# Kernel optimization log

Hardware: AMD Instinct MI355X
Metric: run time of the kernel (lower is better)

Reference implementation:

```python
import jax, jax.numpy as jnp
import numpy as np


def setup_inputs() -> dict:
    key = jax.random.key(0)
    k1, k2, k3 = jax.random.split(key, 3)
    B, N, L, H, E = 4, 4, 1024, 8, 64
    queries = jax.random.normal(k1, (B, N, L, H, E), dtype=jnp.float32)
    keys = jax.random.normal(k2, (B, N, L, H, E), dtype=jnp.float32)
    values = jax.random.normal(k3, (B, N, L, H, E), dtype=jnp.float32)
    return {"queries": queries, "keys": keys, "values": values}


def reference(queries, keys, values):
    B, N, L, H, E = queries.shape
    S = values.shape[2]
    scale = 1.0 / jnp.sqrt(jnp.asarray(E, queries.dtype))
    # scores: [B, N, H, L, S]
    scores = jnp.einsum('bnlhe,bnshe->bnhls', queries, keys)
    # causal mask: True above the diagonal (future positions), broadcast over b,n,h
    causal = jnp.triu(jnp.ones((L, S), dtype=bool), k=1)
    scores = jnp.where(causal, -jnp.inf, scores)
    A = jax.nn.softmax(scale * scores, axis=-1)  # dropout p=0.0 -> identity
    V = jnp.einsum('bnhls,bnshd->bnlhd', A, values)
    return V
```

## Files before the change

### kernel.cpp

```cpp
#include <hip/hip_runtime.h>
#include <hip/hip_bf16.h>


typedef __bf16 bf16x8 __attribute__((ext_vector_type(8)));
typedef float  f32x4  __attribute__((ext_vector_type(4)));

#define SEQ 1024
#define ROWSTRIDE 512
#define LDSPAD 72

__device__ inline bf16x8 pack8(float4 a, float4 b) {
    bf16x8 f;
    f[0]=(__bf16)a.x; f[1]=(__bf16)a.y; f[2]=(__bf16)a.z; f[3]=(__bf16)a.w;
    f[4]=(__bf16)b.x; f[5]=(__bf16)b.y; f[6]=(__bf16)b.z; f[7]=(__bf16)b.w;
    return f;
}

__device__ inline void lds_barrier() {
    asm volatile("s_waitcnt lgkmcnt(0)\n\ts_barrier" ::: "memory");
}

__global__ __launch_bounds__(256) void attn_fwd(
    const float* __restrict__ Qg,
    const float* __restrict__ Kg,
    const float* __restrict__ Vg,
    float* __restrict__ Og)
{
    __shared__ __bf16 Kds[64][LDSPAD];
    __shared__ __bf16 Vds[64][LDSPAD];
    __shared__ __bf16 Pds[2][4][16][LDSPAD];

    const int blk  = blockIdx.x;
    const int pr   = blk >> 7;
    const int head = blk & 127;
    const int h    = head & 7;
    const int bn   = head >> 3;
    const int qts[2] = { pr, 15 - pr };

    const int tid  = threadIdx.x;
    const int wave = tid >> 6;
    const int lane = tid & 63;
    const int quad = lane >> 4;
    const int l15  = lane & 15;

    const size_t base = (size_t)bn * SEQ * ROWSTRIDE + (size_t)h * 64;

    bf16x8 qa[2][2];
    int qrow[2];
    #pragma unroll
    for (int st = 0; st < 2; ++st) {
        qrow[st] = qts[st] * 64 + wave * 16;
        const float* qp = Qg + base + (size_t)(qrow[st] + l15) * ROWSTRIDE + quad * 8;
        #pragma unroll
        for (int t = 0; t < 2; ++t)
            qa[st][t] = pack8(*(const float4*)(qp + t * 32),
                              *(const float4*)(qp + t * 32 + 4));
    }

    f32x4 o[2][4];
    float lsum[2][4];
    #pragma unroll
    for (int st = 0; st < 2; ++st) {
        #pragma unroll
        for (int e = 0; e < 4; ++e) o[st][e] = (f32x4){0.f, 0.f, 0.f, 0.f};
        #pragma unroll
        for (int r = 0; r < 4; ++r) lsum[st][r] = 0.f;
    }

    const float kscale = 0.125f * 1.44269504088896f;

    const int sr = tid >> 2, sc = (tid & 3) << 4;
    const int ve = tid & 63, vs = (tid >> 6) << 4;

    const int ntiles = qts[1] + 1;

    const float* kbase = Kg + base;
    const float* vbase = Vg + base;

    float4 kpre[4];
    float  vpre[16];
    {
        const float* kp = kbase + (size_t)sr * ROWSTRIDE + sc;
        #pragma unroll
        for (int i = 0; i < 4; ++i) kpre[i] = *(const float4*)(kp + i * 4);
        const float* vp = vbase + (size_t)vs * ROWSTRIDE + ve;
        #pragma unroll
        for (int j = 0; j < 16; ++j) vpre[j] = vp[(size_t)j * ROWSTRIDE];
    }

    for (int tile = 0; tile < ntiles; ++tile) {
        lds_barrier();

        *(bf16x8*)&Kds[sr][sc]     = pack8(kpre[0], kpre[1]);
        *(bf16x8*)&Kds[sr][sc + 8] = pack8(kpre[2], kpre[3]);
        {
            bf16x8 f0, f1;
            #pragma unroll
            for (int jj = 0; jj < 8; ++jj) { f0[jj] = (__bf16)vpre[jj]; f1[jj] = (__bf16)vpre[8 + jj]; }
            *(bf16x8*)&Vds[ve][vs]     = f0;
            *(bf16x8*)&Vds[ve][vs + 8] = f1;
        }

        if (tile + 1 < ntiles) {
            const int s0n = (tile + 1) * 64;
            const float* kp = kbase + (size_t)(s0n + sr) * ROWSTRIDE + sc;
            #pragma unroll
            for (int i = 0; i < 4; ++i) kpre[i] = *(const float4*)(kp + i * 4);
            const float* vp = vbase + (size_t)(s0n + vs) * ROWSTRIDE + ve;
            #pragma unroll
            for (int j = 0; j < 16; ++j) vpre[j] = vp[(size_t)j * ROWSTRIDE];
        }

        lds_barrier();

        #pragma unroll
        for (int st = 0; st < 2; ++st) {
            if (tile > qts[st]) continue;
            f32x4 sacc[4];
            #pragma unroll
            for (int c = 0; c < 4; ++c) {
                sacc[c] = (f32x4){0.f, 0.f, 0.f, 0.f};
                #pragma unroll
                for (int t = 0; t < 2; ++t) {
                    bf16x8 kb = *(const bf16x8*)&Kds[c * 16 + l15][t * 32 + quad * 8];
                    sacc[c] = __builtin_amdgcn_mfma_f32_16x16x32_bf16(qa[st][t], kb, sacc[c], 0, 0, 0);
                }
            }
            const bool diag = (tile == qts[st]);
            #pragma unroll
            for (int c = 0; c < 4; ++c) {
                #pragma unroll
                for (int r = 0; r < 4; ++r) {
                    float x = sacc[c][r] * kscale;
                    if (diag && (c * 16 + l15 > wave * 16 + quad * 4 + r)) x = -1e30f;
                    float p = exp2f(x);
                    lsum[st][r] += p;
                    Pds[st][wave][quad * 4 + r][c * 16 + l15] = (__bf16)p;
                }
            }
        }

        asm volatile("s_waitcnt lgkmcnt(0)" ::: "memory");

        const bool both = (tile <= qts[0]);
        #pragma unroll
        for (int e = 0; e < 4; ++e) {
            #pragma unroll
            for (int t = 0; t < 2; ++t) {
                bf16x8 vb = *(const bf16x8*)&Vds[e * 16 + l15][t * 32 + quad * 8];
                if (both) {
                    bf16x8 pa0 = *(const bf16x8*)&Pds[0][wave][l15][t * 32 + quad * 8];
                    o[0][e] = __builtin_amdgcn_mfma_f32_16x16x32_bf16(pa0, vb, o[0][e], 0, 0, 0);
                }
                bf16x8 pa1 = *(const bf16x8*)&Pds[1][wave][l15][t * 32 + quad * 8];
                o[1][e] = __builtin_amdgcn_mfma_f32_16x16x32_bf16(pa1, vb, o[1][e], 0, 0, 0);
            }
        }
    }

    #pragma unroll
    for (int st = 0; st < 2; ++st) {
        float inv_l[4];
        #pragma unroll
        for (int r = 0; r < 4; ++r) {
            float s = lsum[st][r];
            #pragma unroll
            for (int off = 1; off < 16; off <<= 1)
                s += __shfl_xor(s, off);
            inv_l[r] = 1.f / s;
        }
        #pragma unroll
        for (int e = 0; e < 4; ++e) {
            #pragma unroll
            for (int r = 0; r < 4; ++r) {
                size_t oidx = base + (size_t)(qrow[st] + quad * 4 + r) * ROWSTRIDE + e * 16 + l15;
                Og[oidx] = o[st][e][r] * inv_l[r];
            }
        }
    }
}

extern "C" void kernel_launch(void* const* d_in, const int* in_sizes, int n_in,
                              void* d_out, int out_size, void* d_ws, size_t ws_size,
                              hipStream_t stream) {
    const float* Qg = (const float*)d_in[0];
    const float* Kg = (const float*)d_in[1];
    const float* Vg = (const float*)d_in[2];
    float* Og = (float*)d_out;
    attn_fwd<<<dim3(1024), dim3(256), 0, stream>>>(Qg, Kg, Vg, Og);
}
```

Measured before the change: 167.2 us.

## Transpose MFMA operands so each lane owns a query row, vectorize P and output stores

Swaps the A/B operands of both MFMAs so score and output accumulators are transposed, giving each lane a single query row. This lets P be written to LDS as 4-wide bf16 vectors, reduces the row-sum reduction to two shuffles, and turns output stores into float4 writes. The softmax scale is folded into Q at load time and exp2 uses the raw hardware builtin, with masking applied after the exponent. The cost is slightly different rounding from scaling Q before the bf16 conversion, and LDS bank patterns change for the vector P writes.

```diff
diff --git a/kernel.cpp b/kernel.cpp
--- a/kernel.cpp
+++ b/kernel.cpp
@@ -3,6 +3,7 @@
 
 
 typedef __bf16 bf16x8 __attribute__((ext_vector_type(8)));
+typedef __bf16 bf16x4 __attribute__((ext_vector_type(4)));
 typedef float  f32x4  __attribute__((ext_vector_type(4)));
 
 #define SEQ 1024
@@ -13,6 +14,13 @@
     bf16x8 f;
     f[0]=(__bf16)a.x; f[1]=(__bf16)a.y; f[2]=(__bf16)a.z; f[3]=(__bf16)a.w;
     f[4]=(__bf16)b.x; f[5]=(__bf16)b.y; f[6]=(__bf16)b.z; f[7]=(__bf16)b.w;
+    return f;
+}
+
+__device__ inline bf16x8 pack8s(float4 a, float4 b, float s) {
+    bf16x8 f;
+    f[0]=(__bf16)(a.x*s); f[1]=(__bf16)(a.y*s); f[2]=(__bf16)(a.z*s); f[3]=(__bf16)(a.w*s);
+    f[4]=(__bf16)(b.x*s); f[5]=(__bf16)(b.y*s); f[6]=(__bf16)(b.z*s); f[7]=(__bf16)(b.w*s);
     return f;
 }
 
@@ -45,6 +53,8 @@
 
     const size_t base = (size_t)bn * SEQ * ROWSTRIDE + (size_t)h * 64;
 
+    const float kscale = 0.125f * 1.44269504088896f;
+
     bf16x8 qa[2][2];
     int qrow[2];
     #pragma unroll
@@ -53,21 +63,18 @@
         const float* qp = Qg + base + (size_t)(qrow[st] + l15) * ROWSTRIDE + quad * 8;
         #pragma unroll
         for (int t = 0; t < 2; ++t)
-            qa[st][t] = pack8(*(const float4*)(qp + t * 32),
-                              *(const float4*)(qp + t * 32 + 4));
+            qa[st][t] = pack8s(*(const float4*)(qp + t * 32),
+                               *(const float4*)(qp + t * 32 + 4), kscale);
     }
 
     f32x4 o[2][4];
-    float lsum[2][4];
+    float lsum[2];
     #pragma unroll
     for (int st = 0; st < 2; ++st) {
         #pragma unroll
         for (int e = 0; e < 4; ++e) o[st][e] = (f32x4){0.f, 0.f, 0.f, 0.f};
-        #pragma unroll
-        for (int r = 0; r < 4; ++r) lsum[st][r] = 0.f;
+        lsum[st] = 0.f;
     }
-
-    const float kscale = 0.125f * 1.44269504088896f;
 
     const int sr = tid >> 2, sc = (tid & 3) << 4;
     const int ve = tid & 63, vs = (tid >> 6) << 4;
@@ -123,21 +130,25 @@
                 #pragma unroll
                 for (int t = 0; t < 2; ++t) {
                     bf16x8 kb = *(const bf16x8*)&Kds[c * 16 + l15][t * 32 + quad * 8];
-                    sacc[c] = __builtin_amdgcn_mfma_f32_16x16x32_bf16(qa[st][t], kb, sacc[c], 0, 0, 0);
+                    sacc[c] = __builtin_amdgcn_mfma_f32_16x16x32_bf16(kb, qa[st][t], sacc[c], 0, 0, 0);
                 }
             }
             const bool diag = (tile == qts[st]);
+            const int qin = wave * 16 + l15;
+            float ls = 0.f;
             #pragma unroll
             for (int c = 0; c < 4; ++c) {
+                bf16x4 pk;
                 #pragma unroll
                 for (int r = 0; r < 4; ++r) {
-                    float x = sacc[c][r] * kscale;
-                    if (diag && (c * 16 + l15 > wave * 16 + quad * 4 + r)) x = -1e30f;
-                    float p = exp2f(x);
-                    lsum[st][r] += p;
-                    Pds[st][wave][quad * 4 + r][c * 16 + l15] = (__bf16)p;
+                    float p = __builtin_amdgcn_exp2f(sacc[c][r]);
+                    if (diag && (c * 16 + quad * 4 + r > qin)) p = 0.f;
+                    ls += p;
+                    pk[r] = (__bf16)p;
                 }
+                *(bf16x4*)&Pds[st][wave][l15][c * 16 + quad * 4] = pk;
             }
+            lsum[st] += ls;
         }
 
         asm volatile("s_waitcnt lgkmcnt(0)" ::: "memory");
@@ -149,33 +160,30 @@
             for (int t = 0; t < 2; ++t) {
                 bf16x8 vb = *(const bf16x8*)&Vds[e * 16 + l15][t * 32 + quad * 8];
                 if (both) {
-                    bf16x8 pa0 = *(const bf16x8*)&Pds[0][wave][l15][t * 32 + quad * 8];
-                    o[0][e] = __builtin_amdgcn_mfma_f32_16x16x32_bf16(pa0, vb, o[0][e], 0, 0, 0);
+                    bf16x8 pb0 = *(const bf16x8*)&Pds[0][wave][l15][t * 32 + quad * 8];
+                    o[0][e] = __builtin_amdgcn_mfma_f32_16x16x32_bf16(vb, pb0, o[0][e], 0, 0, 0);
                 }
-                bf16x8 pa1 = *(const bf16x8*)&Pds[1][wave][l15][t * 32 + quad * 8];
-                o[1][e] = __builtin_amdgcn_mfma_f32_16x16x32_bf16(pa1, vb, o[1][e], 0, 0, 0);
+                bf16x8 pb1 = *(const bf16x8*)&Pds[1][wave][l15][t * 32 + quad * 8];
+                o[1][e] = __builtin_amdgcn_mfma_f32_16x16x32_bf16(vb, pb1, o[1][e], 0, 0, 0);
             }
         }
     }
 
     #pragma unroll
     for (int st = 0; st < 2; ++st) {
-        float inv_l[4];
-        #pragma unroll
-        for (int r = 0; r < 4; ++r) {
-            float s = lsum[st][r];
-            #pragma unroll
-            for (int off = 1; off < 16; off <<= 1)
-                s += __shfl_xor(s, off);
-            inv_l[r] = 1.f / s;
-        }
+        float s = lsum[st];
+        s += __shfl_xor(s, 16);
+        s += __shfl_xor(s, 32);
+        const float inv_l = 1.f / s;
+        float* op = Og + base + (size_t)(qrow[st] + l15) * ROWSTRIDE + quad * 4;
         #pragma unroll
         for (int e = 0; e < 4; ++e) {
-            #pragma unroll
-            for (int r = 0; r < 4; ++r) {
-                size_t oidx = base + (size_t)(qrow[st] + quad * 4 + r) * ROWSTRIDE + e * 16 + l15;
-                Og[oidx] = o[st][e][r] * inv_l[r];
-            }
+            float4 v;
+            v.x = o[st][e][0] * inv_l;
+            v.y = o[st][e][1] * inv_l;
+            v.z = o[st][e][2] * inv_l;
+            v.w = o[st][e][3] * inv_l;
+            *(float4*)(op + e * 16) = v;
         }
     }
 }
```

Measured after the change: 162.4 us. 1.03x faster.
